# Optimization experiments

Hardware: AMD Instinct MI355X
Metric: run time of the kernel (lower is better)

The kernel has to match this reference:

```python
import jax, jax.numpy as jnp
import numpy as np

B, T, F, H = 64, 512, 512, 1024


def setup_inputs() -> dict:
    key = jax.random.key(0)
    k1, k2, k3 = jax.random.split(key, 3)
    x = jax.random.normal(k1, (B, T, F), dtype=jnp.float32)
    c0 = jnp.zeros((B, H), dtype=jnp.float32)
    h0 = jnp.zeros((B, H), dtype=jnp.float32)
    # Flax LSTMCell: input projection (no bias) + hidden projection (with bias),
    # fused here into [4H]-wide kernels with gate order (i, f, g, o).
    Wi = jax.random.normal(k2, (F, 4 * H), dtype=jnp.float32) / np.sqrt(F)
    Wh = jax.random.normal(k3, (H, 4 * H), dtype=jnp.float32) / np.sqrt(H)
    bh = jnp.zeros((4 * H,), dtype=jnp.float32)
    return {"x": x, "c0": c0, "h0": h0, "Wi": Wi, "Wh": Wh, "bh": bh}


def reference(x, c0, h0, Wi, Wh, bh):
    # Precompute input projections for the whole sequence in one big GEMM.
    # zx: (T, B, 4H)
    zx = jnp.einsum('btf,fg->tbg', x, Wi)

    def step(carry, zx_t):
        c, h = carry
        z = zx_t + h @ Wh + bh  # (B, 4H)
        i, f, g, o = jnp.split(z, 4, axis=-1)
        i = jax.nn.sigmoid(i)
        f = jax.nn.sigmoid(f)
        g = jnp.tanh(g)
        o = jax.nn.sigmoid(o)
        c_new = f * c + i * g
        h_new = o * jnp.tanh(c_new)
        return (c_new, h_new), h_new

    (_, _), ys = jax.lax.scan(step, (c0, h0), zx)
    return jnp.swapaxes(ys, 0, 1)  # (B, T, H)
```

## Files before the change

### kernel.cpp

```cpp
#include <hip/hip_runtime.h>

#define Bdim 64
#define Tdim 512
#define Fdim 512
#define Hdim 1024
#define NKB  48
#define NXKB 16
#define NHKB 32
#define NWG  128
#define NTHR 256

typedef __attribute__((ext_vector_type(8))) _Float16            f16x8;
typedef __attribute__((ext_vector_type(4))) float               f32x4;

#define MFMA(a, b, c) __builtin_amdgcn_mfma_f32_16x16x32_f16((a), (b), (c), 0, 0, 0)

#define WP_ELEMS  (256*48*64*8)
#define BIAS_OFF  ((size_t)WP_ELEMS * 2)
#define HBUF_OFF  (BIAS_OFF + 4096 * 4)
#define HBUF_HALF 65536
#define FLAG_OFF  (HBUF_OFF + (size_t)2 * HBUF_HALF * 2)
#define FLAG_STRIDE 32

__device__ __forceinline__ float sigmoidf_(float v) {
    return 1.0f / (1.0f + __expf(-v));
}
__device__ __forceinline__ float tanhf_(float v) {
    return 1.0f - 2.0f / (1.0f + __expf(2.0f * v));
}

__device__ __forceinline__ f16x8 uload16(const void* p) {
    f16x8 r;
    asm volatile("global_load_dwordx4 %0, %1, off sc0 sc1"
                 : "=v"(r) : "v"(p) : "memory");
    return r;
}

#define WAITV(N) do { asm volatile("s_waitcnt vmcnt(" #N ")" ::: "memory"); \
                      __builtin_amdgcn_sched_barrier(0); } while (0)

__global__ void pack_w_kernel(const float* __restrict__ Wi, const float* __restrict__ Wh,
                              _Float16* __restrict__ Wp)
{
    int d = blockIdx.x * blockDim.x + threadIdx.x;
    int tn   = d / 3072;
    int r    = d % 3072;
    int kb   = r / 64;
    int lane = r % 64;
    int kg = lane >> 4, lm = lane & 15;
    int Np = tn * 16 + lm;
    int g    = Np >> 5;
    int lc   = Np & 31;
    int gate = lc >> 3, c = lc & 7;
    int n  = gate * Hdim + g * 8 + c;
    int k0 = kb * 32 + kg * 8;
    f16x8 v;
#pragma unroll
    for (int j = 0; j < 8; ++j) {
        int k = k0 + j;
        float w = (k < Fdim) ? Wi[(long)k * 4096 + n] : Wh[(long)(k - Fdim) * 4096 + n];
        v[j] = (_Float16)w;
    }
    ((f16x8*)Wp)[d] = v;
}

__global__ void pack_misc_kernel(const float* __restrict__ bh, const float* __restrict__ h0,
                                 float* __restrict__ bias_p, _Float16* __restrict__ hbuf,
                                 unsigned int* __restrict__ flags)
{
    int t = blockIdx.x * blockDim.x + threadIdx.x;
    if (t < NWG) flags[t * FLAG_STRIDE] = 0u;
    if (t < 4096) {
        int g = t >> 5, lc = t & 31;
        int gate = lc >> 3, c = lc & 7;
        bias_p[t] = bh[gate * Hdim + g * 8 + c];
    }
    {
        int wgp = t >> 9;
        int b   = (t >> 3) & 63;
        int c   = t & 7;
        hbuf[t] = (_Float16)h0[b * Hdim + wgp * 8 + c];
    }
}

__global__ __launch_bounds__(NTHR, 1)
void lstm_kernel(const float* __restrict__ x, const float* __restrict__ c0,
                 const f16x8* __restrict__ Wp8, const float* __restrict__ bias_p,
                 _Float16* __restrict__ hbuf, unsigned int* __restrict__ flags,
                 float* __restrict__ out)
{
    __shared__ f16x8 wlds[2 * NKB * 64];
    __shared__ float zlds[Bdim][33];

    const int wg   = (blockIdx.x & 7) * 16 + (blockIdx.x >> 3);
    const int tid  = threadIdx.x;
    const int wave = tid >> 6;
    const int lane = tid & 63;
    const int kg = lane >> 4;
    const int lm = lane & 15;

    {
        const f16x8* src = Wp8 + (size_t)wg * 2 * NKB * 64;
        for (int e = tid; e < 2 * NKB * 64; e += NTHR) wlds[e] = src[e];
    }

    const float bias0 = bias_p[wg * 32 + lm];
    const float bias1 = bias_p[wg * 32 + 16 + lm];

    const int grow = wave * 16 + (lane >> 2);
    const int gjl  = (lane & 3) * 2;
    float cc0 = c0[grow * Hdim + wg * 8 + gjl];
    float cc1 = c0[grow * Hdim + wg * 8 + gjl + 1];

    const int arow = wave * 16 + lm;
    const float* __restrict__ xrow = x + (size_t)arow * Tdim * Fdim + kg * 8;

    const char* __restrict__ hrdbase =
        (const char*)hbuf + (size_t)kg * 1024 + (size_t)arow * 16;

    __syncthreads();

    for (int t = 0; t < Tdim; ++t) {
        const int cur = t & 1;

        f32x4 acc0a = {bias0, bias0, bias0, bias0};
        f32x4 acc1a = {bias1, bias1, bias1, bias1};
        f32x4 acc0b = {0.f, 0.f, 0.f, 0.f};
        f32x4 acc1b = {0.f, 0.f, 0.f, 0.f};

        {
            const float* xt = xrow + (size_t)t * Fdim;
#pragma unroll 8
            for (int kb = 0; kb < NXKB; ++kb) {
                const f32x4* ap = (const f32x4*)(xt + kb * 32);
                f32x4 lo = ap[0];
                f32x4 hi = ap[1];
                f16x8 a;
#pragma unroll
                for (int j = 0; j < 4; ++j) { a[j] = (_Float16)lo[j]; a[4 + j] = (_Float16)hi[j]; }
                f16x8 bf0 = wlds[kb * 64 + lane];
                f16x8 bf1 = wlds[NKB * 64 + kb * 64 + lane];
                if (kb & 1) { acc0b = MFMA(a, bf0, acc0b); acc1b = MFMA(a, bf1, acc1b); }
                else        { acc0a = MFMA(a, bf0, acc0a); acc1a = MFMA(a, bf1, acc1a); }
            }
        }

        if (t && wave == 0) {
            const unsigned int gen = (unsigned int)t;
            while (true) {
                unsigned int f0 = __hip_atomic_load(flags + (size_t)lane * FLAG_STRIDE,
                                                    __ATOMIC_RELAXED, __HIP_MEMORY_SCOPE_AGENT);
                unsigned int f1 = __hip_atomic_load(flags + (size_t)(64 + lane) * FLAG_STRIDE,
                                                    __ATOMIC_RELAXED, __HIP_MEMORY_SCOPE_AGENT);
                if (__all(f0 >= gen && f1 >= gen)) break;
                __builtin_amdgcn_s_sleep(2);
            }
        }
        __syncthreads();

        {
            const char* hq = hrdbase + (size_t)cur * (HBUF_HALF * 2);
            f16x8 hA[8], hB[8];
            WAITV(0);

#define HLOAD(BASE, H)                                                  \
            _Pragma("unroll")                                           \
            for (int k = 0; k < 8; ++k)                                 \
                H[k] = uload16(hq + (size_t)((BASE) + k) * 4096);

#define HGROUP(BASE, H)                                                 \
            _Pragma("unroll")                                           \
            for (int k = 0; k < 8; ++k) {                               \
                int kb = (BASE) + k;                                    \
                f16x8 bf0 = wlds[(NXKB + kb) * 64 + lane];              \
                f16x8 bf1 = wlds[NKB * 64 + (NXKB + kb) * 64 + lane];   \
                if (kb & 1) { acc0b = MFMA(H[k], bf0, acc0b); acc1b = MFMA(H[k], bf1, acc1b); } \
                else        { acc0a = MFMA(H[k], bf0, acc0a); acc1a = MFMA(H[k], bf1, acc1a); } \
            }

            HLOAD(0,  hA);
            HLOAD(8,  hB);
            WAITV(8);
            HGROUP(0,  hA);
            HLOAD(16, hA);
            WAITV(8);
            HGROUP(8,  hB);
            HLOAD(24, hB);
            WAITV(8);
            HGROUP(16, hA);
            WAITV(0);
            HGROUP(24, hB);
#undef HLOAD
#undef HGROUP
        }
        f32x4 z0 = acc0a + acc0b;
        f32x4 z1 = acc1a + acc1b;

        {
            int rbase = wave * 16 + kg * 4;
#pragma unroll
            for (int r = 0; r < 4; ++r) {
                zlds[rbase + r][lm]      = z0[r];
                zlds[rbase + r][16 + lm] = z1[r];
            }
        }
        asm volatile("s_waitcnt lgkmcnt(0)" ::: "memory");
        __builtin_amdgcn_sched_barrier(0);

        float hv0, hv1;
        {
            float i0 = sigmoidf_(zlds[grow][gjl]);
            float f0 = sigmoidf_(zlds[grow][8 + gjl]);
            float g0 = tanhf_(zlds[grow][16 + gjl]);
            float o0 = sigmoidf_(zlds[grow][24 + gjl]);
            cc0 = f0 * cc0 + i0 * g0;
            hv0 = o0 * tanhf_(cc0);

            float i1 = sigmoidf_(zlds[grow][gjl + 1]);
            float f1 = sigmoidf_(zlds[grow][8 + gjl + 1]);
            float g1 = tanhf_(zlds[grow][16 + gjl + 1]);
            float o1 = sigmoidf_(zlds[grow][24 + gjl + 1]);
            cc1 = f1 * cc1 + i1 * g1;
            hv1 = o1 * tanhf_(cc1);
        }

        {
            union { _Float16 h[2]; unsigned int u; } pk;
            pk.h[0] = (_Float16)hv0; pk.h[1] = (_Float16)hv1;
            unsigned int nbu = __shfl(pk.u, lane ^ 1);
            if (!(lane & 1)) {
                unsigned long long v = (unsigned long long)pk.u
                                     | ((unsigned long long)nbu << 32);
                __hip_atomic_store((unsigned long long*)
                    (hbuf + (size_t)(cur ^ 1) * HBUF_HALF + (size_t)wg * 512
                          + (size_t)grow * 8 + gjl),
                    v, __ATOMIC_RELAXED, __HIP_MEMORY_SCOPE_AGENT);
            }
        }
        asm volatile("s_waitcnt vmcnt(0)" ::: "memory");
        __syncthreads();
        if (tid == 0)
            __hip_atomic_store(flags + (size_t)wg * FLAG_STRIDE, (unsigned int)(t + 1),
                               __ATOMIC_RELAXED, __HIP_MEMORY_SCOPE_AGENT);

        {
            float2 ov; ov.x = hv0; ov.y = hv1;
            *(float2*)(out + ((size_t)grow * Tdim + t) * Hdim + wg * 8 + gjl) = ov;
        }
    }
}

extern "C" void kernel_launch(void* const* d_in, const int* in_sizes, int n_in,
                              void* d_out, int out_size, void* d_ws, size_t ws_size,
                              hipStream_t stream)
{
    const float* x  = (const float*)d_in[0];
    const float* c0 = (const float*)d_in[1];
    const float* h0 = (const float*)d_in[2];
    const float* Wi = (const float*)d_in[3];
    const float* Wh = (const float*)d_in[4];
    const float* bh = (const float*)d_in[5];
    float* out = (float*)d_out;

    char* ws = (char*)d_ws;
    _Float16*     Wp     = (_Float16*)(ws);
    float*        bias_p = (float*)(ws + BIAS_OFF);
    _Float16*     hbuf   = (_Float16*)(ws + HBUF_OFF);
    unsigned int* flags  = (unsigned int*)(ws + FLAG_OFF);

    hipLaunchKernelGGL(pack_w_kernel,    dim3(3072), dim3(256), 0, stream, Wi, Wh, Wp);
    hipLaunchKernelGGL(pack_misc_kernel, dim3(256),  dim3(256), 0, stream, bh, h0, bias_p, hbuf, flags);
    hipLaunchKernelGGL(lstm_kernel, dim3(NWG), dim3(NTHR), 0, stream,
                       x, c0, (const f16x8*)Wp, bias_p, hbuf, flags, out);
}
```

Measured before the change: 3.584 ms.

## Replace flag-based grid barrier with sentinel-tagged data polling over 4 slots

After: 3.637 ms. About the same (+1.5%).

```diff
diff --git a/kernel.cpp b/kernel.cpp
--- a/kernel.cpp
+++ b/kernel.cpp
@@ -9,18 +9,19 @@
 #define NHKB 32
 #define NWG  128
 #define NTHR 256
-
-typedef __attribute__((ext_vector_type(8))) _Float16            f16x8;
-typedef __attribute__((ext_vector_type(4))) float               f32x4;
+#define NSLOT 4
+
+typedef __attribute__((ext_vector_type(8))) _Float16     f16x8;
+typedef __attribute__((ext_vector_type(4))) float        f32x4;
+typedef __attribute__((ext_vector_type(4))) unsigned int u32x4;
 
 #define MFMA(a, b, c) __builtin_amdgcn_mfma_f32_16x16x32_f16((a), (b), (c), 0, 0, 0)
 
-#define WP_ELEMS  (256*48*64*8)
-#define BIAS_OFF  ((size_t)WP_ELEMS * 2)
-#define HBUF_OFF  (BIAS_OFF + 4096 * 4)
-#define HBUF_HALF 65536
-#define FLAG_OFF  (HBUF_OFF + (size_t)2 * HBUF_HALF * 2)
-#define FLAG_STRIDE 32
+#define WP_ELEMS    (256*48*64*8)
+#define BIAS_OFF    ((size_t)WP_ELEMS * 2)
+#define HBUF_OFF    (BIAS_OFF + 4096 * 4)
+#define SLOT_HALVES 65536
+#define SLOT_BYTES  131072
 
 __device__ __forceinline__ float sigmoidf_(float v) {
     return 1.0f / (1.0f + __expf(-v));
@@ -35,9 +36,19 @@
                  : "=v"(r) : "v"(p) : "memory");
     return r;
 }
+__device__ __forceinline__ void ustore16(void* p, f32x4 v) {
+    asm volatile("global_store_dwordx4 %0, %1, off sc0 sc1"
+                 :: "v"(p), "v"(v) : "memory");
+}
 
 #define WAITV(N) do { asm volatile("s_waitcnt vmcnt(" #N ")" ::: "memory"); \
                       __builtin_amdgcn_sched_barrier(0); } while (0)
+
+__device__ __forceinline__ bool stale8(f16x8 v) {
+    u32x4 u = __builtin_bit_cast(u32x4, v);
+    return (u[0] == 0xFFFFFFFFu) | (u[1] == 0xFFFFFFFFu) |
+           (u[2] == 0xFFFFFFFFu) | (u[3] == 0xFFFFFFFFu);
+}
 
 __global__ void pack_w_kernel(const float* __restrict__ Wi, const float* __restrict__ Wh,
                               _Float16* __restrict__ Wp)
@@ -65,11 +76,9 @@
 }
 
 __global__ void pack_misc_kernel(const float* __restrict__ bh, const float* __restrict__ h0,
-                                 float* __restrict__ bias_p, _Float16* __restrict__ hbuf,
-                                 unsigned int* __restrict__ flags)
+                                 float* __restrict__ bias_p, _Float16* __restrict__ hbuf)
 {
     int t = blockIdx.x * blockDim.x + threadIdx.x;
-    if (t < NWG) flags[t * FLAG_STRIDE] = 0u;
     if (t < 4096) {
         int g = t >> 5, lc = t & 31;
         int gate = lc >> 3, c = lc & 7;
@@ -81,13 +90,17 @@
         int c   = t & 7;
         hbuf[t] = (_Float16)h0[b * Hdim + wgp * 8 + c];
     }
+    {
+        unsigned int* up = (unsigned int*)(hbuf + SLOT_HALVES);
+        up[t] = 0xFFFFFFFFu;
+        if (t < 32768) up[65536 + t] = 0xFFFFFFFFu;
+    }
 }
 
 __global__ __launch_bounds__(NTHR, 1)
 void lstm_kernel(const float* __restrict__ x, const float* __restrict__ c0,
                  const f16x8* __restrict__ Wp8, const float* __restrict__ bias_p,
-                 _Float16* __restrict__ hbuf, unsigned int* __restrict__ flags,
-                 float* __restrict__ out)
+                 _Float16* __restrict__ hbuf, float* __restrict__ out)
 {
     __shared__ f16x8 wlds[2 * NKB * 64];
     __shared__ float zlds[Bdim][33];
@@ -115,13 +128,22 @@
     const int arow = wave * 16 + lm;
     const float* __restrict__ xrow = x + (size_t)arow * Tdim * Fdim + kg * 8;
 
-    const char* __restrict__ hrdbase =
-        (const char*)hbuf + (size_t)kg * 1024 + (size_t)arow * 16;
+    char* __restrict__ hb  = (char*)hbuf;
+    const char* __restrict__ hrd = hb + (size_t)kg * 1024 + (size_t)arow * 16;
+    const size_t mypkt = (size_t)wg * 1024 + (size_t)grow * 16;
 
     __syncthreads();
 
     for (int t = 0; t < Tdim; ++t) {
-        const int cur = t & 1;
+        const int slot  = t & 3;
+        const int wslot = (t + 1) & 3;
+        const int cslot = (t + 2) & 3;
+
+        if (!(lane & 3)) {
+            u32x4 sv = {0xFFFFFFFFu, 0xFFFFFFFFu, 0xFFFFFFFFu, 0xFFFFFFFFu};
+            ustore16(hb + (size_t)cslot * SLOT_BYTES + mypkt,
+                     __builtin_bit_cast(f32x4, sv));
+        }
 
         f32x4 acc0a = {bias0, bias0, bias0, bias0};
         f32x4 acc1a = {bias1, bias1, bias1, bias1};
@@ -145,28 +167,32 @@
             }
         }
 
-        if (t && wave == 0) {
-            const unsigned int gen = (unsigned int)t;
-            while (true) {
-                unsigned int f0 = __hip_atomic_load(flags + (size_t)lane * FLAG_STRIDE,
-                                                    __ATOMIC_RELAXED, __HIP_MEMORY_SCOPE_AGENT);
-                unsigned int f1 = __hip_atomic_load(flags + (size_t)(64 + lane) * FLAG_STRIDE,
-                                                    __ATOMIC_RELAXED, __HIP_MEMORY_SCOPE_AGENT);
-                if (__all(f0 >= gen && f1 >= gen)) break;
-                __builtin_amdgcn_s_sleep(2);
-            }
-        }
-        __syncthreads();
-
-        {
-            const char* hq = hrdbase + (size_t)cur * (HBUF_HALF * 2);
+        {
+            const char* hq = hrd + (size_t)slot * SLOT_BYTES;
             f16x8 hA[8], hB[8];
-            WAITV(0);
 
 #define HLOAD(BASE, H)                                                  \
             _Pragma("unroll")                                           \
             for (int k = 0; k < 8; ++k)                                 \
                 H[k] = uload16(hq + (size_t)((BASE) + k) * 4096);
+
+#define HCHECK(BASE, H)                                                 \
+            {                                                           \
+                bool st[8]; bool any = false;                           \
+                _Pragma("unroll")                                       \
+                for (int k = 0; k < 8; ++k) { st[k] = stale8(H[k]); any |= st[k]; } \
+                while (__any(any)) {                                    \
+                    __builtin_amdgcn_s_sleep(1);                        \
+                    _Pragma("unroll")                                   \
+                    for (int k = 0; k < 8; ++k)                         \
+                        if (st[k]) H[k] = uload16(hq + (size_t)((BASE) + k) * 4096); \
+                    asm volatile("s_waitcnt vmcnt(0)" ::: "memory");    \
+                    __builtin_amdgcn_sched_barrier(0);                  \
+                    any = false;                                        \
+                    _Pragma("unroll")                                   \
+                    for (int k = 0; k < 8; ++k) { st[k] = stale8(H[k]); any |= st[k]; } \
+                }                                                       \
+            }
 
 #define HGROUP(BASE, H)                                                 \
             _Pragma("unroll")                                           \
@@ -181,16 +207,21 @@
             HLOAD(0,  hA);
             HLOAD(8,  hB);
             WAITV(8);
+            HCHECK(0,  hA);
             HGROUP(0,  hA);
             HLOAD(16, hA);
             WAITV(8);
+            HCHECK(8,  hB);
             HGROUP(8,  hB);
             HLOAD(24, hB);
             WAITV(8);
+            HCHECK(16, hA);
             HGROUP(16, hA);
             WAITV(0);
+            HCHECK(24, hB);
             HGROUP(24, hB);
 #undef HLOAD
+#undef HCHECK
 #undef HGROUP
         }
         f32x4 z0 = acc0a + acc0b;
@@ -227,21 +258,17 @@
         {
             union { _Float16 h[2]; unsigned int u; } pk;
             pk.h[0] = (_Float16)hv0; pk.h[1] = (_Float16)hv1;
-            unsigned int nbu = __shfl(pk.u, lane ^ 1);
-            if (!(lane & 1)) {
-                unsigned long long v = (unsigned long long)pk.u
-                                     | ((unsigned long long)nbu << 32);
-                __hip_atomic_store((unsigned long long*)
-                    (hbuf + (size_t)(cur ^ 1) * HBUF_HALF + (size_t)wg * 512
-                          + (size_t)grow * 8 + gjl),
-                    v, __ATOMIC_RELAXED, __HIP_MEMORY_SCOPE_AGENT);
-            }
-        }
-        asm volatile("s_waitcnt vmcnt(0)" ::: "memory");
-        __syncthreads();
-        if (tid == 0)
-            __hip_atomic_store(flags + (size_t)wg * FLAG_STRIDE, (unsigned int)(t + 1),
-                               __ATOMIC_RELAXED, __HIP_MEMORY_SCOPE_AGENT);
+            const int lb = lane & ~3;
+            unsigned int q0 = __shfl(pk.u, lb);
+            unsigned int q1 = __shfl(pk.u, lb + 1);
+            unsigned int q2 = __shfl(pk.u, lb + 2);
+            unsigned int q3 = __shfl(pk.u, lb + 3);
+            if (!(lane & 3)) {
+                u32x4 pkt = {q0, q1, q2, q3};
+                ustore16(hb + (size_t)wslot * SLOT_BYTES + mypkt,
+                         __builtin_bit_cast(f32x4, pkt));
+            }
+        }
 
         {
             float2 ov; ov.x = hv0; ov.y = hv1;
@@ -263,13 +290,12 @@
     float* out = (float*)d_out;
 
     char* ws = (char*)d_ws;
-    _Float16*     Wp     = (_Float16*)(ws);
-    float*        bias_p = (float*)(ws + BIAS_OFF);
-    _Float16*     hbuf   = (_Float16*)(ws + HBUF_OFF);
-    unsigned int* flags  = (unsigned int*)(ws + FLAG_OFF);
+    _Float16* Wp     = (_Float16*)(ws);
+    float*    bias_p = (float*)(ws + BIAS_OFF);
+    _Float16* hbuf   = (_Float16*)(ws + HBUF_OFF);
 
     hipLaunchKernelGGL(pack_w_kernel,    dim3(3072), dim3(256), 0, stream, Wi, Wh, Wp);
-    hipLaunchKernelGGL(pack_misc_kernel, dim3(256),  dim3(256), 0, stream, bh, h0, bias_p, hbuf, flags);
+    hipLaunchKernelGGL(pack_misc_kernel, dim3(256),  dim3(256), 0, stream, bh, h0, bias_p, hbuf);
     hipLaunchKernelGGL(lstm_kernel, dim3(NWG), dim3(NTHR), 0, stream,
-                       x, c0, (const f16x8*)Wp, bias_p, hbuf, flags, out);
-}
+                       x, c0, (const f16x8*)Wp, bias_p, hbuf, out);
+}
```

## Use per-step h ring buffer with per-wave flag increments and L2-cached loads

Applied to the files above, without the earlier changes.

Result: faster. 3.380 ms (-5.7%).

```diff
diff --git a/kernel.cpp b/kernel.cpp
--- a/kernel.cpp
+++ b/kernel.cpp
@@ -10,16 +10,18 @@
 #define NWG  128
 #define NTHR 256
 
-typedef __attribute__((ext_vector_type(8))) _Float16            f16x8;
-typedef __attribute__((ext_vector_type(4))) float               f32x4;
+typedef __attribute__((ext_vector_type(8))) _Float16     f16x8;
+typedef __attribute__((ext_vector_type(4))) float        f32x4;
+typedef __attribute__((ext_vector_type(4))) unsigned int u32x4;
 
 #define MFMA(a, b, c) __builtin_amdgcn_mfma_f32_16x16x32_f16((a), (b), (c), 0, 0, 0)
 
-#define WP_ELEMS  (256*48*64*8)
-#define BIAS_OFF  ((size_t)WP_ELEMS * 2)
-#define HBUF_OFF  (BIAS_OFF + 4096 * 4)
-#define HBUF_HALF 65536
-#define FLAG_OFF  (HBUF_OFF + (size_t)2 * HBUF_HALF * 2)
+#define WP_ELEMS    (256*48*64*8)
+#define BIAS_OFF    ((size_t)WP_ELEMS * 2)
+#define HBUF_OFF    (BIAS_OFF + 4096 * 4)
+#define SLOT_BYTES  131072
+#define NRING       513
+#define FLAG_OFF    (HBUF_OFF + (size_t)NRING * SLOT_BYTES)
 #define FLAG_STRIDE 32
 
 __device__ __forceinline__ float sigmoidf_(float v) {
@@ -29,11 +31,15 @@
     return 1.0f - 2.0f / (1.0f + __expf(2.0f * v));
 }
 
-__device__ __forceinline__ f16x8 uload16(const void* p) {
+__device__ __forceinline__ f16x8 uload16_l2(const void* p) {
     f16x8 r;
-    asm volatile("global_load_dwordx4 %0, %1, off sc0 sc1"
+    asm volatile("global_load_dwordx4 %0, %1, off sc0"
                  : "=v"(r) : "v"(p) : "memory");
     return r;
+}
+__device__ __forceinline__ void ustore16(void* p, f32x4 v) {
+    asm volatile("global_store_dwordx4 %0, %1, off sc0 sc1"
+                 :: "v"(p), "v"(v) : "memory");
 }
 
 #define WAITV(N) do { asm volatile("s_waitcnt vmcnt(" #N ")" ::: "memory"); \
@@ -115,13 +121,14 @@
     const int arow = wave * 16 + lm;
     const float* __restrict__ xrow = x + (size_t)arow * Tdim * Fdim + kg * 8;
 
-    const char* __restrict__ hrdbase =
-        (const char*)hbuf + (size_t)kg * 1024 + (size_t)arow * 16;
+    char* __restrict__ hb  = (char*)hbuf;
+    const char* __restrict__ hrd = hb + (size_t)kg * 1024 + (size_t)arow * 16;
+    const size_t mypkt = (size_t)wg * 1024 + (size_t)grow * 16;
 
     __syncthreads();
 
     for (int t = 0; t < Tdim; ++t) {
-        const int cur = t & 1;
+        const unsigned int gen = (unsigned int)t;
 
         f32x4 acc0a = {bias0, bias0, bias0, bias0};
         f32x4 acc1a = {bias1, bias1, bias1, bias1};
@@ -146,27 +153,26 @@
         }
 
         if (t && wave == 0) {
-            const unsigned int gen = (unsigned int)t;
+            const unsigned int target = 4u * gen;
             while (true) {
                 unsigned int f0 = __hip_atomic_load(flags + (size_t)lane * FLAG_STRIDE,
                                                     __ATOMIC_RELAXED, __HIP_MEMORY_SCOPE_AGENT);
                 unsigned int f1 = __hip_atomic_load(flags + (size_t)(64 + lane) * FLAG_STRIDE,
                                                     __ATOMIC_RELAXED, __HIP_MEMORY_SCOPE_AGENT);
-                if (__all(f0 >= gen && f1 >= gen)) break;
-                __builtin_amdgcn_s_sleep(2);
+                if (__all(f0 >= target && f1 >= target)) break;
+                __builtin_amdgcn_s_sleep(1);
             }
         }
         __syncthreads();
 
         {
-            const char* hq = hrdbase + (size_t)cur * (HBUF_HALF * 2);
+            const char* hq = hrd + (size_t)t * SLOT_BYTES;
             f16x8 hA[8], hB[8];
-            WAITV(0);
 
 #define HLOAD(BASE, H)                                                  \
             _Pragma("unroll")                                           \
             for (int k = 0; k < 8; ++k)                                 \
-                H[k] = uload16(hq + (size_t)((BASE) + k) * 4096);
+                H[k] = uload16_l2(hq + (size_t)((BASE) + k) * 4096);
 
 #define HGROUP(BASE, H)                                                 \
             _Pragma("unroll")                                           \
@@ -227,21 +233,21 @@
         {
             union { _Float16 h[2]; unsigned int u; } pk;
             pk.h[0] = (_Float16)hv0; pk.h[1] = (_Float16)hv1;
-            unsigned int nbu = __shfl(pk.u, lane ^ 1);
-            if (!(lane & 1)) {
-                unsigned long long v = (unsigned long long)pk.u
-                                     | ((unsigned long long)nbu << 32);
-                __hip_atomic_store((unsigned long long*)
-                    (hbuf + (size_t)(cur ^ 1) * HBUF_HALF + (size_t)wg * 512
-                          + (size_t)grow * 8 + gjl),
-                    v, __ATOMIC_RELAXED, __HIP_MEMORY_SCOPE_AGENT);
+            const int lb = lane & ~3;
+            unsigned int q0 = __shfl(pk.u, lb);
+            unsigned int q1 = __shfl(pk.u, lb + 1);
+            unsigned int q2 = __shfl(pk.u, lb + 2);
+            unsigned int q3 = __shfl(pk.u, lb + 3);
+            if (!(lane & 3)) {
+                u32x4 pkt = {q0, q1, q2, q3};
+                ustore16(hb + (size_t)(t + 1) * SLOT_BYTES + mypkt,
+                         __builtin_bit_cast(f32x4, pkt));
             }
         }
         asm volatile("s_waitcnt vmcnt(0)" ::: "memory");
-        __syncthreads();
-        if (tid == 0)
-            __hip_atomic_store(flags + (size_t)wg * FLAG_STRIDE, (unsigned int)(t + 1),
-                               __ATOMIC_RELAXED, __HIP_MEMORY_SCOPE_AGENT);
+        if (lane == 0)
+            __hip_atomic_fetch_add(flags + (size_t)wg * FLAG_STRIDE, 1u,
+                                   __ATOMIC_RELAXED, __HIP_MEMORY_SCOPE_AGENT);
 
         {
             float2 ov; ov.x = hv0; ov.y = hv1;
```
